# Kernel tuning notes

Hardware: AMD Instinct MI355X
Metric: run time of the kernel (lower is better)

The kernel has to match this reference:

```python
import jax, jax.numpy as jnp
import numpy as np

B, S, IN, OUT, SPLIT = 4, 2048, 4096, 4096, 1024


def setup_inputs() -> dict:
    key = jax.random.key(0)
    ks = jax.random.split(key, 14)
    def n(k, shape, scale=1.0):
        return jax.random.normal(k, shape, dtype=jnp.float32) * scale
    return {
        "x": n(ks[0], (B, S, IN)),
        "V": n(ks[1], (SPLIT, IN)),
        "U": n(ks[2], (OUT, SPLIT)),
        "v2": n(ks[3], (1, IN), 0.05),
        "v1": n(ks[4], (1, SPLIT), 0.05),
        "u2": n(ks[5], (1, SPLIT), 0.05),
        "u1": n(ks[6], (1, OUT), 0.05),
        "V_R": n(ks[7], (SPLIT, IN)),
        "U_R": n(ks[8], (OUT, SPLIT)),
        "v2_R": n(ks[9], (1, IN), 0.05),
        "v1_R": n(ks[10], (1, SPLIT), 0.05),
        "u2_R": n(ks[11], (1, SPLIT), 0.05),
        "u1_R": n(ks[12], (1, OUT), 0.05),
        "bias": n(ks[13], (OUT,), 0.02),
    }


def _quantize(w):
    # ITQ binarization: sign(w) with straight-through estimator semantics
    return w + jax.lax.stop_gradient(jnp.sign(w) - w)


def _compute_forward(x2d, V, U, v2, v1, u2, u1):
    # x2d: [T, in]; V: [split, in]; U: [out, split]
    Vq = _quantize(V)
    Uq = _quantize(U)
    v1u2 = v1 * u2  # [1, split]
    h = (x2d * v2) @ Vq.T          # [T, split]
    return (h * v1u2) @ Uq.T * u1  # [T, out]


def reference(x, V, U, v2, v1, u2, u1, V_R, U_R, v2_R, v1_R, u2_R, u1_R, bias):
    lead = x.shape[:-1]
    x2d = x.reshape(-1, x.shape[-1])
    y = _compute_forward(x2d, V, U, v2, v1, u2, u1)
    y = y + _compute_forward(x2d, V_R, U_R, v2_R, v1_R, u2_R, u1_R)
    y = y + bias
    return y.reshape(lead + (U.shape[0],))
```

## Files before the change

### kernel.cpp

```cpp
#include <hip/hip_runtime.h>


typedef __bf16 bf16x8 __attribute__((ext_vector_type(8)));
typedef float floatx4 __attribute__((ext_vector_type(4)));

__device__ __forceinline__ unsigned short f2bf_rne(float f) {
    union { float f; unsigned u; } v; v.f = f;
    unsigned r = v.u + 0x7FFFu + ((v.u >> 16) & 1u);
    return (unsigned short)(r >> 16);
}

__device__ __forceinline__ float sgnf(float w) {
    return (float)((w > 0.f) - (w < 0.f));
}

__device__ __forceinline__ void async_copy16(const void* g, void* l) {
    __builtin_amdgcn_global_load_lds(
        (const __attribute__((address_space(1))) void*)g,
        (__attribute__((address_space(3))) void*)l, 16, 0, 0);
}


__global__ void cast_x_kernel(const float* __restrict__ x,
                              unsigned short* __restrict__ xb, int n4) {
    int i = blockIdx.x * blockDim.x + threadIdx.x;
    if (i >= n4) return;
    float4 v = ((const float4*)x)[i];
    ushort4 o;
    o.x = f2bf_rne(v.x); o.y = f2bf_rne(v.y);
    o.z = f2bf_rne(v.z); o.w = f2bf_rne(v.w);
    ((ushort4*)xb)[i] = o;
}

__global__ void prep_w_kernel(const float* __restrict__ V, const float* __restrict__ V_R,
                              const float* __restrict__ v2, const float* __restrict__ v2_R,
                              const float* __restrict__ U, const float* __restrict__ U_R,
                              const float* __restrict__ v1, const float* __restrict__ v1_R,
                              const float* __restrict__ u2, const float* __restrict__ u2_R,
                              const float* __restrict__ u1, const float* __restrict__ u1_R,
                              unsigned short* __restrict__ W1,
                              unsigned short* __restrict__ W2) {
    int bid = blockIdx.x;
    if (bid < 8192) {
        int i = bid * blockDim.x + threadIdx.x;
        int idx = i << 2;
        int scat = idx >> 12;
        int k = idx & 4095;
        const float* Vp; const float* sp;
        if (scat < 1024) { Vp = V + ((size_t)scat << 12); sp = v2; }
        else             { Vp = V_R + ((size_t)(scat - 1024) << 12); sp = v2_R; }
        float4 w = *(const float4*)(Vp + k);
        float4 s = *(const float4*)(sp + k);
        ushort4 o;
        o.x = f2bf_rne(sgnf(w.x) * s.x);
        o.y = f2bf_rne(sgnf(w.y) * s.y);
        o.z = f2bf_rne(sgnf(w.z) * s.z);
        o.w = f2bf_rne(sgnf(w.w) * s.w);
        ((ushort4*)W1)[i] = o;
    } else {
        int i = (bid - 8192) * blockDim.x + threadIdx.x;
        int idx = i << 2;
        int o = idx >> 11;
        int scat = idx & 2047;
        int branch = scat >> 10;
        int s = scat & 1023;
        const float* Up  = branch ? U_R  : U;
        const float* v1p = branch ? v1_R : v1;
        const float* u2p = branch ? u2_R : u2;
        float u1v = (branch ? u1_R : u1)[o];
        float4 w = *(const float4*)(Up + ((size_t)o << 10) + s);
        float4 a = *(const float4*)(v1p + s);
        float4 b = *(const float4*)(u2p + s);
        ushort4 out;
        out.x = f2bf_rne(sgnf(w.x) * a.x * b.x * u1v);
        out.y = f2bf_rne(sgnf(w.y) * a.y * b.y * u1v);
        out.z = f2bf_rne(sgnf(w.z) * a.z * b.z * u1v);
        out.w = f2bf_rne(sgnf(w.w) * a.w * b.w * u1v);
        ((ushort4*)W2)[i] = out;
    }
}


template <bool OUT_BF16, bool ADD_BIAS>
__global__ void gemm_bt(const unsigned short* __restrict__ A,
                        const unsigned short* __restrict__ B,
                        void* __restrict__ Cv,
                        const float* __restrict__ bias,
                        int M, int N, int K) {
    __shared__ __align__(16) unsigned short As[128 * 64];
    __shared__ __align__(16) unsigned short Bs[128 * 64];

    const int tid = threadIdx.x;
    const int wave = tid >> 6;
    const int lane = tid & 63;
    const int m0 = blockIdx.x * 128;
    const int n0 = blockIdx.y * 128;

    const int lrow = lane >> 3;
    const int lcol = (((lane & 7) ^ lrow)) << 3;

    const int wm = (wave >> 1) << 6;
    const int wn = (wave & 1) << 6;
    const int fm = lane & 15;
    const int rk = lane & 7;
    const int cgl = lane >> 4;

    floatx4 acc[4][4];
#pragma unroll
    for (int i = 0; i < 4; ++i)
#pragma unroll
        for (int j = 0; j < 4; ++j)
#pragma unroll
            for (int r = 0; r < 4; ++r) acc[i][j][r] = 0.f;

    const size_t Ks = (size_t)K;
    for (int k0 = 0; k0 < K; k0 += 64) {
#pragma unroll
        for (int i = 0; i < 4; ++i) {
            const int row = wave * 32 + i * 8;
            const unsigned short* gA = A + (size_t)(m0 + row + lrow) * Ks + (k0 + lcol);
            const unsigned short* gB = B + (size_t)(n0 + row + lrow) * Ks + (k0 + lcol);
            async_copy16(gA, &As[row * 64]);
            async_copy16(gB, &Bs[row * 64]);
        }
        __syncthreads();
#pragma unroll
        for (int ks = 0; ks < 64; ks += 32) {
            const int cg = (ks >> 3) | cgl;
            const int roff = (cg ^ rk) << 3;
            bf16x8 af[4], bfr[4];
#pragma unroll
            for (int i = 0; i < 4; ++i)
                af[i] = *(const bf16x8*)&As[(wm + i * 16 + fm) * 64 + roff];
#pragma unroll
            for (int i = 0; i < 4; ++i)
                bfr[i] = *(const bf16x8*)&Bs[(wn + i * 16 + fm) * 64 + roff];
#pragma unroll
            for (int mi = 0; mi < 4; ++mi)
#pragma unroll
                for (int ni = 0; ni < 4; ++ni)
                    acc[mi][ni] = __builtin_amdgcn_mfma_f32_16x16x32_bf16(
                        af[mi], bfr[ni], acc[mi][ni], 0, 0, 0);
        }
        __syncthreads();
    }

    const int rq = (lane >> 4) << 2;
    const int col = lane & 15;
#pragma unroll
    for (int mi = 0; mi < 4; ++mi) {
#pragma unroll
        for (int r = 0; r < 4; ++r) {
            const int gm = m0 + wm + mi * 16 + rq + r;
            const size_t base = (size_t)gm * (size_t)N;
#pragma unroll
            for (int ni = 0; ni < 4; ++ni) {
                const int gn = n0 + wn + ni * 16 + col;
                float v = acc[mi][ni][r];
                if (ADD_BIAS) v += bias[gn];
                if (OUT_BF16)
                    ((unsigned short*)Cv)[base + gn] = f2bf_rne(v);
                else
                    ((float*)Cv)[base + gn] = v;
            }
        }
    }
}


extern "C" void kernel_launch(void* const* d_in, const int* in_sizes, int n_in,
                              void* d_out, int out_size, void* d_ws, size_t ws_size,
                              hipStream_t stream) {
    const float* x    = (const float*)d_in[0];
    const float* V    = (const float*)d_in[1];
    const float* U    = (const float*)d_in[2];
    const float* v2   = (const float*)d_in[3];
    const float* v1   = (const float*)d_in[4];
    const float* u2   = (const float*)d_in[5];
    const float* u1   = (const float*)d_in[6];
    const float* V_R  = (const float*)d_in[7];
    const float* U_R  = (const float*)d_in[8];
    const float* v2_R = (const float*)d_in[9];
    const float* v1_R = (const float*)d_in[10];
    const float* u2_R = (const float*)d_in[11];
    const float* u1_R = (const float*)d_in[12];
    const float* bias = (const float*)d_in[13];
    float* out = (float*)d_out;

    char* ws = (char*)d_ws;
    unsigned short* Xb = (unsigned short*)ws;
    unsigned short* W1 = (unsigned short*)(ws + (size_t)67108864);
    unsigned short* W2 = (unsigned short*)(ws + (size_t)67108864 + 16777216);
    unsigned short* H  = (unsigned short*)(ws + (size_t)67108864 + 33554432);

    cast_x_kernel<<<32768, 256, 0, stream>>>(x, Xb, 8388608);
    prep_w_kernel<<<16384, 256, 0, stream>>>(V, V_R, v2, v2_R,
                                             U, U_R, v1, v1_R, u2, u2_R, u1, u1_R,
                                             W1, W2);

    gemm_bt<true, false><<<dim3(64, 16), 256, 0, stream>>>(Xb, W1, (void*)H, nullptr, 8192, 2048, 4096);
    gemm_bt<false, true><<<dim3(64, 32), 256, 0, stream>>>(H, W2, (void*)out, bias, 8192, 4096, 2048);
}
```

Before: 546.7 us.

## Double-buffer GEMM LDS tiles and merge prep kernels into one launch

The GEMM now uses two LDS buffers for the A and B tiles. It issues the async global-to-LDS copy for the next K-tile before computing on the current one, and needs only one barrier per iteration, so loads overlap MFMA work. The x cast and the weight preparation kernels are merged into a single launch to save one kernel launch. In exchange, LDS per block doubles to 64KB, which can lower the number of resident blocks per CU.

```diff
diff --git a/kernel.cpp b/kernel.cpp
--- a/kernel.cpp
+++ b/kernel.cpp
@@ -20,29 +20,25 @@
         (__attribute__((address_space(3))) void*)l, 16, 0, 0);
 }
 
-
-__global__ void cast_x_kernel(const float* __restrict__ x,
-                              unsigned short* __restrict__ xb, int n4) {
-    int i = blockIdx.x * blockDim.x + threadIdx.x;
-    if (i >= n4) return;
-    float4 v = ((const float4*)x)[i];
-    ushort4 o;
-    o.x = f2bf_rne(v.x); o.y = f2bf_rne(v.y);
-    o.z = f2bf_rne(v.z); o.w = f2bf_rne(v.w);
-    ((ushort4*)xb)[i] = o;
-}
-
-__global__ void prep_w_kernel(const float* __restrict__ V, const float* __restrict__ V_R,
-                              const float* __restrict__ v2, const float* __restrict__ v2_R,
-                              const float* __restrict__ U, const float* __restrict__ U_R,
-                              const float* __restrict__ v1, const float* __restrict__ v1_R,
-                              const float* __restrict__ u2, const float* __restrict__ u2_R,
-                              const float* __restrict__ u1, const float* __restrict__ u1_R,
-                              unsigned short* __restrict__ W1,
-                              unsigned short* __restrict__ W2) {
+__global__ void prep_all_kernel(const float* __restrict__ x, unsigned short* __restrict__ Xb,
+                                const float* __restrict__ V, const float* __restrict__ V_R,
+                                const float* __restrict__ v2, const float* __restrict__ v2_R,
+                                const float* __restrict__ U, const float* __restrict__ U_R,
+                                const float* __restrict__ v1, const float* __restrict__ v1_R,
+                                const float* __restrict__ u2, const float* __restrict__ u2_R,
+                                const float* __restrict__ u1, const float* __restrict__ u1_R,
+                                unsigned short* __restrict__ W1,
+                                unsigned short* __restrict__ W2) {
     int bid = blockIdx.x;
-    if (bid < 8192) {
+    if (bid < 32768) {
         int i = bid * blockDim.x + threadIdx.x;
+        float4 v = ((const float4*)x)[i];
+        ushort4 o;
+        o.x = f2bf_rne(v.x); o.y = f2bf_rne(v.y);
+        o.z = f2bf_rne(v.z); o.w = f2bf_rne(v.w);
+        ((ushort4*)Xb)[i] = o;
+    } else if (bid < 40960) {
+        int i = (bid - 32768) * blockDim.x + threadIdx.x;
         int idx = i << 2;
         int scat = idx >> 12;
         int k = idx & 4095;
@@ -58,7 +54,7 @@
         o.w = f2bf_rne(sgnf(w.w) * s.w);
         ((ushort4*)W1)[i] = o;
     } else {
-        int i = (bid - 8192) * blockDim.x + threadIdx.x;
+        int i = (bid - 40960) * blockDim.x + threadIdx.x;
         int idx = i << 2;
         int o = idx >> 11;
         int scat = idx & 2047;
@@ -82,13 +78,14 @@
 
 
 template <bool OUT_BF16, bool ADD_BIAS>
-__global__ void gemm_bt(const unsigned short* __restrict__ A,
-                        const unsigned short* __restrict__ B,
-                        void* __restrict__ Cv,
-                        const float* __restrict__ bias,
-                        int M, int N, int K) {
-    __shared__ __align__(16) unsigned short As[128 * 64];
-    __shared__ __align__(16) unsigned short Bs[128 * 64];
+__global__ __launch_bounds__(256)
+void gemm_bt(const unsigned short* __restrict__ A,
+             const unsigned short* __restrict__ B,
+             void* __restrict__ Cv,
+             const float* __restrict__ bias,
+             int M, int N, int K) {
+    __shared__ __align__(16) unsigned short As[2][128 * 64];
+    __shared__ __align__(16) unsigned short Bs[2][128 * 64];
 
     const int tid = threadIdx.x;
     const int wave = tid >> 6;
@@ -114,16 +111,27 @@
             for (int r = 0; r < 4; ++r) acc[i][j][r] = 0.f;
 
     const size_t Ks = (size_t)K;
+    const int srow = wave * 32;
+
+#pragma unroll
+    for (int i = 0; i < 4; ++i) {
+        const int row = srow + i * 8;
+        async_copy16(A + (size_t)(m0 + row + lrow) * Ks + lcol, &As[0][row * 64]);
+        async_copy16(B + (size_t)(n0 + row + lrow) * Ks + lcol, &Bs[0][row * 64]);
+    }
+    __syncthreads();
+
+    int p = 0;
     for (int k0 = 0; k0 < K; k0 += 64) {
-#pragma unroll
-        for (int i = 0; i < 4; ++i) {
-            const int row = wave * 32 + i * 8;
-            const unsigned short* gA = A + (size_t)(m0 + row + lrow) * Ks + (k0 + lcol);
-            const unsigned short* gB = B + (size_t)(n0 + row + lrow) * Ks + (k0 + lcol);
-            async_copy16(gA, &As[row * 64]);
-            async_copy16(gB, &Bs[row * 64]);
+        if (k0 + 64 < K) {
+            const int kn = k0 + 64;
+#pragma unroll
+            for (int i = 0; i < 4; ++i) {
+                const int row = srow + i * 8;
+                async_copy16(A + (size_t)(m0 + row + lrow) * Ks + (kn + lcol), &As[1 - p][row * 64]);
+                async_copy16(B + (size_t)(n0 + row + lrow) * Ks + (kn + lcol), &Bs[1 - p][row * 64]);
+            }
         }
-        __syncthreads();
 #pragma unroll
         for (int ks = 0; ks < 64; ks += 32) {
             const int cg = (ks >> 3) | cgl;
@@ -131,10 +139,10 @@
             bf16x8 af[4], bfr[4];
 #pragma unroll
             for (int i = 0; i < 4; ++i)
-                af[i] = *(const bf16x8*)&As[(wm + i * 16 + fm) * 64 + roff];
+                af[i] = *(const bf16x8*)&As[p][(wm + i * 16 + fm) * 64 + roff];
 #pragma unroll
             for (int i = 0; i < 4; ++i)
-                bfr[i] = *(const bf16x8*)&Bs[(wn + i * 16 + fm) * 64 + roff];
+                bfr[i] = *(const bf16x8*)&Bs[p][(wn + i * 16 + fm) * 64 + roff];
 #pragma unroll
             for (int mi = 0; mi < 4; ++mi)
 #pragma unroll
@@ -143,6 +151,7 @@
                         af[mi], bfr[ni], acc[mi][ni], 0, 0, 0);
         }
         __syncthreads();
+        p ^= 1;
     }
 
     const int rq = (lane >> 4) << 2;
@@ -193,10 +202,9 @@
     unsigned short* W2 = (unsigned short*)(ws + (size_t)67108864 + 16777216);
     unsigned short* H  = (unsigned short*)(ws + (size_t)67108864 + 33554432);
 
-    cast_x_kernel<<<32768, 256, 0, stream>>>(x, Xb, 8388608);
-    prep_w_kernel<<<16384, 256, 0, stream>>>(V, V_R, v2, v2_R,
-                                             U, U_R, v1, v1_R, u2, u2_R, u1, u1_R,
-                                             W1, W2);
+    prep_all_kernel<<<49152, 256, 0, stream>>>(x, Xb, V, V_R, v2, v2_R,
+                                               U, U_R, v1, v1_R, u2, u2_R, u1, u1_R,
+                                               W1, W2);
 
     gemm_bt<true, false><<<dim3(64, 16), 256, 0, stream>>>(Xb, W1, (void*)H, nullptr, 8192, 2048, 4096);
     gemm_bt<false, true><<<dim3(64, 32), 256, 0, stream>>>(H, W2, (void*)out, bias, 8192, 4096, 2048);
```

Result: slower. 596.5 us (+9.1%).
